# Optimization experiments

Hardware: AMD Instinct MI355X
Metric: run time of the kernel (lower is better)

The kernel has to match this reference:

```python
import jax, jax.numpy as jnp
import numpy as np

N, C, T, V = 32, 64, 512, 21
INTER = 16  # out_channels // coff_embedding(4)
EPS = 1e-5


def _build_A():
    # 21-joint skeleton, spatial strategy: [self(identity), inward, outward], column-normalized
    parents = [-1, 0, 1, 2, 3, 1, 5, 6, 1, 8, 9, 0, 11, 12, 13, 0, 15, 16, 17, 7, 10]
    inw = np.zeros((V, V), np.float32)
    for i, p in enumerate(parents):
        if p >= 0:
            inw[i, p] = 1.0

    def norm(a):
        d = a.sum(0)
        return a * np.where(d > 0, 1.0 / d, 0.0).astype(np.float32)

    I = np.eye(V, dtype=np.float32)
    return np.stack([norm(I), norm(inw), norm(inw.T)]).astype(np.float32)


def setup_inputs():
    key = jax.random.key(0)
    k = jax.random.split(key, 24)
    rn = lambda i, s: jax.random.normal(k[i], s, jnp.float32)
    A = jnp.asarray(_build_A())
    return dict(
        x=rn(0, (N, C, T, V)),
        A=A,
        bn1_gamma=1.0 + 0.1 * rn(1, (C * V,)),
        bn1_beta=0.1 * rn(2, (C * V,)),
        bn1_mean=0.05 * rn(3, (C * V,)),
        bn1_var=jnp.ones((C * V,), jnp.float32),
        PA=A,
        alpha=rn(4, (1,)),
        wa=0.05 * rn(5, (3, INTER, C)), ba=0.05 * rn(6, (3, INTER)),
        wb=0.05 * rn(7, (3, INTER, C)), bb=0.05 * rn(8, (3, INTER)),
        wd=0.05 * rn(9, (3, C, C)), bd=0.05 * rn(10, (3, C)),
        bn2_gamma=1.0 + 0.1 * rn(11, (C,)),
        bn2_beta=0.1 * rn(12, (C,)),
        bn2_mean=0.05 * rn(13, (C,)),
        bn2_var=jnp.ones((C,), jnp.float32),
        w_sa=0.05 * rn(14, (1, C, V)), b_sa=0.05 * rn(15, (1,)),
        w_ta=0.05 * rn(16, (1, C, 9)), b_ta=0.05 * rn(17, (1,)),
        w_fc1=0.05 * rn(18, (C // 2, C)), b_fc1=0.05 * rn(19, (C // 2,)),
        w_fc2=0.05 * rn(20, (C, C // 2)), b_fc2=0.05 * rn(21, (C,)),
    )


def _conv1d(z, w, b):
    pad = (w.shape[2] - 1) // 2
    y = jax.lax.conv_general_dilated(z, w, (1,), [(pad, pad)],
                                     dimension_numbers=('NCH', 'OIH', 'NCH'))
    return y + b[None, :, None]


def reference(x, A, bn1_gamma, bn1_beta, bn1_mean, bn1_var, PA, alpha,
              wa, ba, wb, bb, wd, bd, bn2_gamma, bn2_beta, bn2_mean, bn2_var,
              w_sa, b_sa, w_ta, b_ta, w_fc1, b_fc1, w_fc2, b_fc2):
    n, c, t, v = x.shape
    # data_bn: (N,C,T,V) -> (N,V,T,C) -> raw reshape (N,V*C,T), BN1d, back to (N,C,T,V)
    xb = x.transpose(0, 3, 2, 1).reshape(n, v * c, t)
    scale1 = (bn1_gamma / jnp.sqrt(bn1_var + EPS))
    xb = (xb - bn1_mean[None, :, None]) * scale1[None, :, None] + bn1_beta[None, :, None]
    xb = xb.reshape(n, v, c, t).transpose(0, 2, 3, 1)  # (N,C,T,V)

    e = wa.shape[1]
    # attention embeddings, vectorized over the 3 subsets (s)
    a1 = (jnp.einsum('nctv,sec->nsvet', xb, wa) + ba[None, :, None, :, None]).reshape(n, 3, v, e * t)
    a2 = (jnp.einsum('nctv,sec->nsetv', xb, wb) + bb[None, :, :, None, None]).reshape(n, 3, e * t, v)
    attn = jnp.tanh(jnp.matmul(a1, a2) / float(e * t))  # (N,3,V,V)
    adj = PA[None] + attn * alpha[0]
    # graph aggregation: (N,1,C*T,V) @ (N,3,V,V)
    xz = jnp.matmul(xb.reshape(n, 1, c * t, v), adj).reshape(n, 3, c, t, v)
    y = jnp.einsum('nsctv,soc->notv', xz, wd) + bd.sum(0)[None, :, None, None]

    scale2 = (bn2_gamma / jnp.sqrt(bn2_var + EPS))
    y = (y - bn2_mean[None, :, None, None]) * scale2[None, :, None, None] + bn2_beta[None, :, None, None]
    y = jax.nn.relu(y + xb)  # residual (in==out -> identity down)

    # spatial attention
    se = y.mean(2)  # (N,C,V)
    y = y * jax.nn.sigmoid(_conv1d(se, w_sa, b_sa))[:, :, None, :] + y
    # temporal attention
    se = y.mean(3)  # (N,C,T)
    y = y * jax.nn.sigmoid(_conv1d(se, w_ta, b_ta))[:, :, :, None] + y
    # channel attention
    se = y.mean((2, 3))  # (N,C)
    se2 = jax.nn.sigmoid(jax.nn.relu(se @ w_fc1.T + b_fc1) @ w_fc2.T + b_fc2)
    y = y * se2[:, :, None, None] + y
    return jax.nn.relu(y)
```

## Files before the change

kernel.cpp:

```cpp
#include <hip/hip_runtime.h>
#include <hip/hip_bf16.h>
#include <math.h>


#define Nn 32
#define Cc 64
#define Tt 512
#define Vv 21
#define VP 24
#define Ss 3
#define EPSf 1e-5f
#define NCHUNK 16
#define SVV (Ss*Vv*Vv)
#define KSTR 136

typedef __attribute__((ext_vector_type(8))) short short8;
typedef __attribute__((ext_vector_type(4))) float f32x4;

__device__ __forceinline__ float sigm(float x){ return 1.f/(1.f+expf(-x)); }
__device__ __forceinline__ float bf2f(unsigned short u){ return __uint_as_float((unsigned)u << 16); }
__device__ __forceinline__ unsigned short f2bf(float f){
    __hip_bfloat16 h = __float2bfloat16(f);
    return *reinterpret_cast<unsigned short*>(&h);
}

__global__ __launch_bounds__(256) void k_xb(
    const float* __restrict__ x,
    const float* __restrict__ g1, const float* __restrict__ b1,
    const float* __restrict__ mu1, const float* __restrict__ var1,
    unsigned short* __restrict__ xbT)
{
    const int c0 = blockIdx.x & 63;
    const int ah = blockIdx.x >> 6;
    const int n  = blockIdx.y;
    const int tid = threadIdx.x;
    __shared__ float brick[256*24];
    __shared__ float2 pps[32*26];

    const float* xs = x + (size_t)(n*64 + c0)*10752 + ah*5376;
    for (int i = tid; i < 1344; i += 256){
        float4 d = *reinterpret_cast<const float4*>(xs + i*4);
        int f = i*4;
        #pragma unroll
        for (int e = 0; e < 4; ++e){
            int fe = f + e;
            int t = fe / 21;
            int v = fe - t*21;
            brick[t*24 + v] = ((const float*)&d)[e];
        }
    }
    for (int i = tid; i < 768; i += 256){
        int al = i / 24, vp = i % 24;
        float2 p = make_float2(0.f, 0.f);
        if (vp < 21){
            int j = vp*64 + ah*32 + al;
            float sc = g1[j]*rsqrtf(var1[j]+EPSf);
            p.x = sc; p.y = b1[j] - mu1[j]*sc;
        }
        pps[al*26 + vp] = p;
    }
    __syncthreads();

    #pragma unroll
    for (int ii = 0; ii < 3; ++ii){
        int i = tid + ii*256;
        int vp  = i % 24;
        int m   = (i / 24) % 8;
        int agl = i / 192;
        unsigned short pk[8];
        #pragma unroll
        for (int da = 0; da < 8; ++da){
            int al = agl*8 + da;
            float val = 0.f;
            if (vp < 21){
                float xv = brick[(al*8 + m)*24 + vp];
                float2 p = pps[al*26 + vp];
                val = xv*p.x + p.y;
            }
            pk[da] = f2bf(val);
        }
        *reinterpret_cast<uint4*>(
            xbT + ((size_t)((n*512 + c0 + 64*m)*24 + vp))*64 + ah*32 + agl*8) =
            *reinterpret_cast<const uint4*>(pk);
    }
}

__global__ __launch_bounds__(256) void k_wdT(
    const float* __restrict__ wd, const float* __restrict__ bd,
    const float* __restrict__ g2, const float* __restrict__ b2,
    const float* __restrict__ mu2, const float* __restrict__ var2,
    unsigned short* __restrict__ wdF, float4* __restrict__ bn2p)
{
    int i = blockIdx.x*256 + threadIdx.x;
    if (i < 1536){
        int s  = i / 512;
        int w  = (i >> 7) & 3;
        int ks = (i >> 6) & 1;
        int l  = i & 63;
        int o  = 16*w + (l & 15);
        #pragma unroll
        for (int j = 0; j < 8; ++j){
            int c = 32*ks + 8*(l >> 4) + j;
            wdF[(size_t)i*8 + j] = f2bf(wd[(s*64 + o)*64 + c]);
        }
    }
    if (i < 64){
        float bsum = bd[i] + bd[64+i] + bd[128+i];
        float sc = g2[i]*rsqrtf(var2[i]+EPSf);
        bn2p[i] = make_float4(bsum, sc, mu2[i], b2[i]);
    }
}

__global__ __launch_bounds__(256) void k_wab(
    const float* __restrict__ wa, const float* __restrict__ wb,
    unsigned short* __restrict__ wawbF)
{
    int i = blockIdx.x*256 + threadIdx.x;
    if (i >= 768) return;
    int mt = i / 128;
    int ks = (i / 64) & 1;
    int l  = i & 63;
    int e  = l & 15;
    int g  = l >> 4;
    const float* src = (mt < 3) ? wa : wb;
    int s = (mt < 3) ? mt : mt - 3;
    #pragma unroll
    for (int j = 0; j < 8; ++j){
        int c = ks*32 + 8*g + j;
        wawbF[(size_t)i*8 + j] = f2bf(src[(s*16 + e)*64 + c]);
    }
}

__global__ __launch_bounds__(256) void k_attn(
    const unsigned short* __restrict__ xbT,
    const unsigned short* __restrict__ wawbF,
    const float* __restrict__ ba, const float* __restrict__ bb,
    float* __restrict__ part)
{
    const int chunk = blockIdx.x;
    const int n = blockIdx.y;
    const int tid = threadIdx.x;
    const int w  = tid >> 6;
    const int l  = tid & 63;
    const int g  = l >> 4;
    const int ln = l & 15;

    __shared__ unsigned short m1buf[3*32*KSTR];
    __shared__ unsigned short m2buf[3*32*KSTR];

    for (int i = tid; i < 3*8*KSTR; i += 256){
        int s = i / (8*KSTR), r = i % (8*KSTR);
        int off = (s*32 + 24)*KSTR + r;
        m1buf[off] = 0; m2buf[off] = 0;
    }

    short8 aF[6][2];
    float4 bias4[6];
    #pragma unroll
    for (int mt = 0; mt < 6; ++mt){
        #pragma unroll
        for (int ks = 0; ks < 2; ++ks)
            aF[mt][ks] = *reinterpret_cast<const short8*>(wawbF + (size_t)((mt*2+ks)*64 + l)*8);
        const float* bsrc = (mt < 3) ? (ba + mt*16) : (bb + (mt-3)*16);
        bias4[mt] = *reinterpret_cast<const float4*>(bsrc + 4*g);
    }

    f32x4 accB[3];
    #pragma unroll
    for (int q = 0; q < 3; ++q) accB[q] = (f32x4){0.f,0.f,0.f,0.f};

    int colv[3], colt[3];
    #pragma unroll
    for (int q = 0; q < 3; ++q){
        int col = (3*w + q)*16 + ln;
        colt[q] = col / 24;
        colv[q] = col % 24;
    }

    for (int st = 0; st < 4; ++st){
        const int tb = chunk*32 + st*8;
        #pragma unroll
        for (int q = 0; q < 3; ++q){
            const unsigned short* bp = xbT + ((size_t)(n*512 + tb + colt[q])*24 + colv[q])*64;
            short8 b0 = *reinterpret_cast<const short8*>(bp + 8*g);
            short8 b1 = *reinterpret_cast<const short8*>(bp + 32 + 8*g);
            #pragma unroll
            for (int mt = 0; mt < 6; ++mt){
                f32x4 c;
                c[0] = bias4[mt].x; c[1] = bias4[mt].y;
                c[2] = bias4[mt].z; c[3] = bias4[mt].w;
                c = __builtin_amdgcn_mfma_f32_16x16x32_bf16(aF[mt][0], b0, c, 0, 0, 0);
                c = __builtin_amdgcn_mfma_f32_16x16x32_bf16(aF[mt][1], b1, c, 0, 0, 0);
                unsigned short* dst = (mt < 3) ? m1buf : m2buf;
                int s = (mt < 3) ? mt : mt - 3;
                unsigned u0 = (unsigned)f2bf(c[0]) | ((unsigned)f2bf(c[1]) << 16);
                unsigned u1 = (unsigned)f2bf(c[2]) | ((unsigned)f2bf(c[3]) << 16);
                int off = (s*32 + colv[q])*KSTR + colt[q]*16 + 4*g;
                *reinterpret_cast<uint2*>(dst + off) = make_uint2(u0, u1);
            }
        }
        __syncthreads();
        #pragma unroll
        for (int q = 0; q < 3; ++q){
            int ct = 3*w + q;
            int s = ct >> 2, mtile = (ct >> 1) & 1, ntile = ct & 1;
            #pragma unroll
            for (int kk = 0; kk < 4; ++kk){
                short8 a = *reinterpret_cast<const short8*>(&m1buf[(s*32 + mtile*16 + ln)*KSTR + kk*32 + 8*g]);
                short8 b = *reinterpret_cast<const short8*>(&m2buf[(s*32 + ntile*16 + ln)*KSTR + kk*32 + 8*g]);
                accB[q] = __builtin_amdgcn_mfma_f32_16x16x32_bf16(a, b, accB[q], 0, 0, 0);
            }
        }
        __syncthreads();
    }

    float* pout = part + (size_t)(n*NCHUNK + chunk)*SVV;
    #pragma unroll
    for (int q = 0; q < 3; ++q){
        int ct = 3*w + q;
        int s = ct >> 2, mtile = (ct >> 1) & 1, ntile = ct & 1;
        int v = ntile*16 + ln;
        #pragma unroll
        for (int r = 0; r < 4; ++r){
            int u = mtile*16 + 4*g + r;
            if (u < 21 && v < 21)
                pout[s*441 + u*21 + v] = accB[q][r];
        }
    }
}

__global__ void k_adj(const float* __restrict__ part, const float* __restrict__ PA,
                      const float* __restrict__ alpha, float* __restrict__ adj)
{
    int i = blockIdx.x*256 + threadIdx.x;
    if (i >= Nn*SVV) return;
    int n = i / SVV;
    int idx = i % SVV;
    float pre = 0.f;
    for (int ch = 0; ch < NCHUNK; ++ch)
        pre += part[(size_t)(n*NCHUNK+ch)*SVV + idx];
    adj[i] = PA[idx] + tanhf(pre * (1.f/8192.f)) * alpha[0];
}

__global__ __launch_bounds__(256) void k_adjF(const float* __restrict__ adj,
                                              unsigned short* __restrict__ adjF)
{
    int i = blockIdx.x*256 + threadIdx.x;
    if (i >= Nn*Ss*2*64) return;
    int n = i / 384;
    int r = i % 384;
    int s = r / 128;
    int r2 = r % 128;
    int h = r2 >> 6;
    int l = r2 & 63;
    int v = 16*h + (l & 15);
    #pragma unroll
    for (int j = 0; j < 8; ++j){
        int u = 8*(l >> 4) + j;
        float val = (u < 21 && v < 21) ? adj[(size_t)n*SVV + s*441 + u*21 + v] : 0.f;
        adjF[(size_t)i*8 + j] = f2bf(val);
    }
}

__global__ __launch_bounds__(256) void k_y0(
    const unsigned short* __restrict__ xbT,
    const unsigned short* __restrict__ adjF,
    const unsigned short* __restrict__ wdF,
    const float4* __restrict__ bn2p,
    float* __restrict__ y0)
{
    const int n  = blockIdx.y;
    const int t0 = blockIdx.x * 4;
    const int tid = threadIdx.x;
    const int w  = tid >> 6;
    const int l  = tid & 63;
    const int g  = l >> 4;
    const int ln = l & 15;

    __shared__ unsigned short xbuf[64*136];
    __shared__ unsigned short zbuf[128*72];

    {
        int c = tid >> 2, t = tid & 3;
        *reinterpret_cast<uint4*>(&xbuf[c*136 + t*32 + 24]) = make_uint4(0u,0u,0u,0u);
    }
    for (int k = 0; k < 3; ++k){
        int i = tid + k*256;
        int u = i % 24, t = (i/24) & 3, cg = i / 96;
        uint4 d = *reinterpret_cast<const uint4*>(
            xbT + ((size_t)(n*512 + t0 + t)*24 + u)*64 + cg*8);
        const unsigned short* p = reinterpret_cast<const unsigned short*>(&d);
        #pragma unroll
        for (int dc = 0; dc < 8; ++dc)
            xbuf[(cg*8 + dc)*136 + t*32 + u] = p[dc];
    }
    __syncthreads();

    short8 ax[4];
    #pragma unroll
    for (int t = 0; t < 4; ++t)
        ax[t] = *reinterpret_cast<const short8*>(&xbuf[(16*w + ln)*136 + t*32 + 8*g]);

    short8 badj[3][2];
    {
        const unsigned short* ap = adjF + (size_t)n*Ss*2*64*8;
        #pragma unroll
        for (int s = 0; s < 3; ++s)
            #pragma unroll
            for (int h = 0; h < 2; ++h)
                badj[s][h] = *reinterpret_cast<const short8*>(ap + ((s*2 + h)*64 + l)*8);
    }

    f32x4 acc[8];
    #pragma unroll
    for (int ct = 0; ct < 8; ++ct) acc[ct] = (f32x4){0.f,0.f,0.f,0.f};

    for (int s = 0; s < 3; ++s){
        if (s) __syncthreads();
        f32x4 dz[8];
        #pragma unroll
        for (int ct = 0; ct < 8; ++ct)
            dz[ct] = __builtin_amdgcn_mfma_f32_16x16x32_bf16(
                         ax[ct>>1], badj[s][ct&1], (f32x4){0.f,0.f,0.f,0.f}, 0, 0, 0);
        #pragma unroll
        for (int ct = 0; ct < 8; ++ct){
            unsigned u0 = (unsigned)f2bf(dz[ct][0]) | ((unsigned)f2bf(dz[ct][1]) << 16);
            unsigned u1 = (unsigned)f2bf(dz[ct][2]) | ((unsigned)f2bf(dz[ct][3]) << 16);
            int col = (ct >> 1)*32 + (ct & 1)*16 + ln;
            *reinterpret_cast<uint2*>(&zbuf[col*72 + 16*w + 4*g]) = make_uint2(u0, u1);
        }
        __syncthreads();
        short8 aw0 = *reinterpret_cast<const short8*>(wdF + (size_t)(((s*4 + w)*2 + 0)*64 + l)*8);
        short8 aw1 = *reinterpret_cast<const short8*>(wdF + (size_t)(((s*4 + w)*2 + 1)*64 + l)*8);
        #pragma unroll
        for (int ct = 0; ct < 8; ++ct){
            int col = (ct >> 1)*32 + (ct & 1)*16 + ln;
            short8 b0 = *reinterpret_cast<const short8*>(&zbuf[col*72 + 0  + 8*g]);
            short8 b1 = *reinterpret_cast<const short8*>(&zbuf[col*72 + 32 + 8*g]);
            acc[ct] = __builtin_amdgcn_mfma_f32_16x16x32_bf16(aw0, b0, acc[ct], 0, 0, 0);
            acc[ct] = __builtin_amdgcn_mfma_f32_16x16x32_bf16(aw1, b1, acc[ct], 0, 0, 0);
        }
    }

    float4 bp[4];
    #pragma unroll
    for (int r = 0; r < 4; ++r) bp[r] = bn2p[16*w + 4*g + r];
    #pragma unroll
    for (int ct = 0; ct < 8; ++ct){
        const int t  = ct >> 1;
        const int vp = (ct & 1)*16 + ln;
        if (vp < 21){
            #pragma unroll
            for (int r = 0; r < 4; ++r){
                const int o = 16*w + 4*g + r;
                float val = acc[ct][r] + bp[r].x;
                val = (val - bp[r].z)*bp[r].y + bp[r].w;
                val += bf2f(xbuf[o*136 + t*32 + vp]);
                y0[((size_t)(n*64 + o)*512 + t0 + t)*21 + vp] = fmaxf(val, 0.f);
            }
        }
    }
}

__global__ __launch_bounds__(256) void k_M1(const float* __restrict__ y0, float* __restrict__ M1)
{
    const int c = blockIdx.x, n = blockIdx.y, tid = threadIdx.x;
    float a[21];
    #pragma unroll
    for (int v = 0; v < 21; ++v) a[v] = 0.f;
    for (int t = tid; t < Tt; t += 256){
        const float* p = &y0[ ((size_t)(n*Cc+c)*Tt + t)*Vv ];
        #pragma unroll
        for (int v = 0; v < 21; ++v) a[v] += p[v];
    }
    __shared__ float red[256][21];
    #pragma unroll
    for (int v = 0; v < 21; ++v) red[tid][v] = a[v];
    __syncthreads();
    for (int off = 128; off > 0; off >>= 1){
        if (tid < off){
            #pragma unroll
            for (int v = 0; v < 21; ++v) red[tid][v] += red[tid+off][v];
        }
        __syncthreads();
    }
    if (tid < 21) M1[(size_t)(n*Cc+c)*Vv + tid] = red[0][tid];
}

__global__ __launch_bounds__(256) void k_s1(const float* __restrict__ M1, const float* __restrict__ w_sa,
                     const float* __restrict__ b_sa, float* __restrict__ s1)
{
    const int n = blockIdx.x, tid = threadIdx.x;
    __shared__ float m1s[64][22];
    __shared__ float ws[64][22];
    __shared__ float red[12][21];
    for (int i = tid; i < 1344; i += 256){
        int c = i / 21, v = i % 21;
        m1s[c][v] = M1[(size_t)(n*64+c)*21 + v];
        ws[c][v]  = w_sa[i];
    }
    __syncthreads();
    const int v = tid % 21;
    const int cg = tid / 21;
    float sum = 0.f;
    if (tid < 252){
        for (int c = cg; c < 64; c += 12){
            #pragma unroll
            for (int k = 0; k < 21; ++k){
                int src = v + k - 10;
                if (src >= 0 && src < 21)
                    sum += m1s[c][src] * ws[c][k];
            }
        }
        red[cg][v] = sum;
    }
    __syncthreads();
    if (tid < 21){
        float tot = b_sa[0];
        #pragma unroll
        for (int g = 0; g < 12; ++g) tot += red[g][tid] * (1.f/512.f);
        s1[n*Vv + tid] = 1.f + sigm(tot);
    }
}

__global__ __launch_bounds__(256) void k_M2(const float* __restrict__ y0, const float* __restrict__ s1,
                      float* __restrict__ M2)
{
    int t = blockIdx.x*256 + threadIdx.x;
    int nc = blockIdx.y;
    int n = nc >> 6;
    __shared__ float s1s[21];
    if (threadIdx.x < 21) s1s[threadIdx.x] = s1[n*Vv + threadIdx.x];
    __syncthreads();
    const float* p = &y0[ ((size_t)nc*Tt + t)*Vv ];
    float sum = 0.f;
    #pragma unroll
    for (int v = 0; v < 21; ++v) sum += p[v]*s1s[v];
    M2[(size_t)nc*Tt + t] = sum;
}

__global__ __launch_bounds__(256) void k_s2(const float* __restrict__ M2, const float* __restrict__ w_ta,
                      const float* __restrict__ b_ta, float* __restrict__ s2)
{
    const int n = blockIdx.y;
    const int t0 = blockIdx.x * 64;
    const int tid = threadIdx.x;
    __shared__ float m2s[64][72];
    __shared__ float wts[576];
    __shared__ float red[4][64];
    for (int i = tid; i < 64*72; i += 256){
        int c = i / 72, tt = i % 72;
        int src = t0 + tt - 4;
        m2s[c][tt] = (src >= 0 && src < 512) ? M2[(size_t)(n*64+c)*512 + src] : 0.f;
    }
    for (int i = tid; i < 576; i += 256) wts[i] = w_ta[i];
    __syncthreads();
    const int tl = tid & 63;
    const int cg = tid >> 6;
    float sum = 0.f;
    for (int c = cg*16; c < cg*16+16; ++c){
        #pragma unroll
        for (int k = 0; k < 9; ++k)
            sum += m2s[c][tl + k] * wts[c*9 + k];
    }
    red[cg][tl] = sum;
    __syncthreads();
    if (cg == 0){
        float tot = b_ta[0] + (red[0][tl]+red[1][tl]+red[2][tl]+red[3][tl]) * (1.f/21.f);
        s2[n*512 + t0 + tl] = 1.f + sigm(tot);
    }
}

__global__ __launch_bounds__(256) void k_sec(const float* __restrict__ M2, const float* __restrict__ s2,
                      float* __restrict__ sec)
{
    const int c = blockIdx.x, n = blockIdx.y, tid = threadIdx.x;
    const float* row = &M2[(size_t)(n*Cc+c)*Tt];
    const float* s2r = &s2[n*Tt];
    float acc = row[tid]*s2r[tid] + row[tid+256]*s2r[tid+256];
    #pragma unroll
    for (int off = 32; off > 0; off >>= 1)
        acc += __shfl_down(acc, off, 64);
    __shared__ float red[4];
    if ((tid & 63) == 0) red[tid >> 6] = acc;
    __syncthreads();
    if (tid == 0)
        sec[n*Cc + c] = (red[0]+red[1]+red[2]+red[3]) * (1.f/(512.f*21.f));
}

__global__ __launch_bounds__(64) void k_s3fc(const float* __restrict__ sec,
                     const float* __restrict__ w1, const float* __restrict__ bf1,
                     const float* __restrict__ w2, const float* __restrict__ bf2,
                     float* __restrict__ s3)
{
    int n = blockIdx.x, c = threadIdx.x;
    __shared__ float secs[64];
    __shared__ float hh[32];
    secs[c] = sec[n*Cc + c];
    __syncthreads();
    if (c < 32){
        float h = bf1[c];
        #pragma unroll 8
        for (int k = 0; k < 64; ++k) h += w1[c*64+k]*secs[k];
        hh[c] = fmaxf(h, 0.f);
    }
    __syncthreads();
    float o = bf2[c];
    #pragma unroll 8
    for (int k = 0; k < 32; ++k) o += w2[c*32+k]*hh[k];
    s3[n*Cc + c] = 1.f + sigm(o);
}

__global__ __launch_bounds__(256) void k_final(float* __restrict__ y,
    const float* __restrict__ s1, const float* __restrict__ s2, const float* __restrict__ s3)
{
    const int c = blockIdx.x, n = blockIdx.y, tid = threadIdx.x;
    __shared__ float s1s[21];
    __shared__ float s2s[512];
    if (tid < 21) s1s[tid] = s1[n*Vv + tid];
    for (int i = tid; i < 512; i += 256) s2s[i] = s2[n*512 + i];
    __syncthreads();
    const float sc3 = s3[n*Cc + c];
    float* base = y + (size_t)(n*Cc + c)*10752;
    for (int i = tid; i < 2688; i += 256){
        float4 d = *reinterpret_cast<const float4*>(base + i*4);
        float r[4];
        #pragma unroll
        for (int e = 0; e < 4; ++e){
            int f = i*4 + e;
            int t = f / 21;
            int v = f - t*21;
            r[e] = fmaxf(((const float*)&d)[e] * s1s[v] * s2s[t] * sc3, 0.f);
        }
        *reinterpret_cast<float4*>(base + i*4) = make_float4(r[0], r[1], r[2], r[3]);
    }
}

extern "C" void kernel_launch(void* const* d_in, const int* in_sizes, int n_in,
                              void* d_out, int out_size, void* d_ws, size_t ws_size,
                              hipStream_t stream)
{
    const float* x    = (const float*)d_in[0];
    const float* g1   = (const float*)d_in[2];
    const float* b1   = (const float*)d_in[3];
    const float* mu1  = (const float*)d_in[4];
    const float* var1 = (const float*)d_in[5];
    const float* PA   = (const float*)d_in[6];
    const float* alpha= (const float*)d_in[7];
    const float* wa   = (const float*)d_in[8];
    const float* ba   = (const float*)d_in[9];
    const float* wb   = (const float*)d_in[10];
    const float* bb   = (const float*)d_in[11];
    const float* wd   = (const float*)d_in[12];
    const float* bd   = (const float*)d_in[13];
    const float* g2   = (const float*)d_in[14];
    const float* b2   = (const float*)d_in[15];
    const float* mu2  = (const float*)d_in[16];
    const float* var2 = (const float*)d_in[17];
    const float* w_sa = (const float*)d_in[18];
    const float* b_sa = (const float*)d_in[19];
    const float* w_ta = (const float*)d_in[20];
    const float* b_ta = (const float*)d_in[21];
    const float* w_fc1= (const float*)d_in[22];
    const float* b_fc1= (const float*)d_in[23];
    const float* w_fc2= (const float*)d_in[24];
    const float* b_fc2= (const float*)d_in[25];

    unsigned short* xbT = (unsigned short*)d_ws;
    float* fws  = (float*)d_ws + 12582912;
    float* part = fws;
    float* adjw = part + 677376;
    float* M1   = adjw + 42336;
    float* s1   = M1   + 43008;
    float* M2   = s1   + 672;
    float* s2   = M2   + 1048576;
    float* s3   = s2   + 16384;
    float4* bn2p = (float4*)(s3 + 2048);
    unsigned short* wdF   = (unsigned short*)((float*)bn2p + 256);
    unsigned short* adjF  = wdF + 12288;
    unsigned short* wawbF = adjF + 98304;
    float* sec  = (float*)(wawbF + 6144);
    float* y0   = (float*)d_out;

    k_xb  <<<dim3(128, Nn), 256, 0, stream>>>(x, g1,b1,mu1,var1, xbT);
    k_wdT <<<6, 256, 0, stream>>>(wd, bd, g2, b2, mu2, var2, wdF, bn2p);
    k_wab <<<3, 256, 0, stream>>>(wa, wb, wawbF);
    k_attn<<<dim3(NCHUNK, Nn), 256, 0, stream>>>(xbT, wawbF, ba, bb, part);
    k_adj <<<(Nn*SVV + 255)/256, 256, 0, stream>>>(part, PA, alpha, adjw);
    k_adjF<<<48, 256, 0, stream>>>(adjw, adjF);
    k_y0  <<<dim3(Tt/4, Nn), 256, 0, stream>>>(xbT, adjF, wdF, bn2p, y0);
    k_M1  <<<dim3(Cc, Nn), 256, 0, stream>>>(y0, M1);
    k_s1  <<<Nn, 256, 0, stream>>>(M1, w_sa, b_sa, s1);
    k_M2  <<<dim3(Tt/256, Nn*Cc), 256, 0, stream>>>(y0, s1, M2);
    k_s2  <<<dim3(8, Nn), 256, 0, stream>>>(M2, w_ta, b_ta, s2);
    k_sec <<<dim3(Cc, Nn), 256, 0, stream>>>(M2, s2, sec);
    k_s3fc<<<Nn, 64, 0, stream>>>(sec, w_fc1, b_fc1, w_fc2, b_fc2, s3);
    k_final<<<dim3(Cc, Nn), 256, 0, stream>>>(y0, s1, s2, s3);
}
```

Before: 199.2 us.

## Restage k_xb with full-row bf16 LDS brick and 64-channel vectorized stores

The xb normalization/transpose kernel now has each block load a full 10752-float slab (both halves) and store it in shared memory as bf16 in a 32-wide swizzled layout. The BN scale and offset are precomputed for all 64 columns, and 192 threads each write eight 16-byte packed outputs. The goal is to halve the block count, cut shared memory footprint, avoid bank conflicts and make global stores contiguous across a 64-wide row. In exchange, 64 of the 256 threads sit idle in the output phase, and the input is rounded to bf16 before the BN affine is applied, which adds a small precision change.

```diff
diff --git a/kernel.cpp b/kernel.cpp
--- a/kernel.cpp
+++ b/kernel.cpp
@@ -30,58 +30,55 @@
     const float* __restrict__ mu1, const float* __restrict__ var1,
     unsigned short* __restrict__ xbT)
 {
-    const int c0 = blockIdx.x & 63;
-    const int ah = blockIdx.x >> 6;
+    const int c0 = blockIdx.x;
     const int n  = blockIdx.y;
     const int tid = threadIdx.x;
-    __shared__ float brick[256*24];
-    __shared__ float2 pps[32*26];
-
-    const float* xs = x + (size_t)(n*64 + c0)*10752 + ah*5376;
-    for (int i = tid; i < 1344; i += 256){
+    __shared__ unsigned short brick16[512*32];
+    __shared__ float scs[21*65], ofs[21*65];
+
+    for (int j = tid; j < 1344; j += 256){
+        int vp = j >> 6, a = j & 63;
+        float sc = g1[j]*rsqrtf(var1[j]+EPSf);
+        scs[vp*65 + a] = sc;
+        ofs[vp*65 + a] = b1[j] - mu1[j]*sc;
+    }
+    const float* xs = x + (size_t)(n*64 + c0)*10752;
+    for (int i = tid; i < 2688; i += 256){
         float4 d = *reinterpret_cast<const float4*>(xs + i*4);
-        int f = i*4;
         #pragma unroll
         for (int e = 0; e < 4; ++e){
-            int fe = f + e;
-            int t = fe / 21;
-            int v = fe - t*21;
-            brick[t*24 + v] = ((const float*)&d)[e];
-        }
-    }
-    for (int i = tid; i < 768; i += 256){
-        int al = i / 24, vp = i % 24;
-        float2 p = make_float2(0.f, 0.f);
-        if (vp < 21){
-            int j = vp*64 + ah*32 + al;
-            float sc = g1[j]*rsqrtf(var1[j]+EPSf);
-            p.x = sc; p.y = b1[j] - mu1[j]*sc;
-        }
-        pps[al*26 + vp] = p;
-    }
-    __syncthreads();
-
-    #pragma unroll
-    for (int ii = 0; ii < 3; ++ii){
-        int i = tid + ii*256;
-        int vp  = i % 24;
-        int m   = (i / 24) % 8;
-        int agl = i / 192;
-        unsigned short pk[8];
+            int f = i*4 + e;
+            int t = f / 21;
+            int v = f - t*21;
+            brick16[t*32 + ((v + 8*(t>>6)) & 31)] = f2bf(((const float*)&d)[e]);
+        }
+    }
+    __syncthreads();
+
+    if (tid < 192){
+        const int agl = tid & 7;
+        const int vp  = tid >> 3;
+        const bool valid = (vp < 21);
+        float scr[8], ofr[8];
         #pragma unroll
         for (int da = 0; da < 8; ++da){
-            int al = agl*8 + da;
-            float val = 0.f;
-            if (vp < 21){
-                float xv = brick[(al*8 + m)*24 + vp];
-                float2 p = pps[al*26 + vp];
-                val = xv*p.x + p.y;
+            scr[da] = valid ? scs[vp*65 + agl*8 + da] : 0.f;
+            ofr[da] = valid ? ofs[vp*65 + agl*8 + da] : 0.f;
+        }
+        unsigned short* ob = xbT + ((size_t)(n*512 + c0)*24 + vp)*64 + agl*8;
+        #pragma unroll
+        for (int m = 0; m < 8; ++m){
+            unsigned short pk[8];
+            #pragma unroll
+            for (int da = 0; da < 8; ++da){
+                int row = agl*64 + da*8 + m;
+                float xv = bf2f(brick16[row*32 + ((vp + 8*agl) & 31)]);
+                float r = xv*scr[da] + ofr[da];
+                pk[da] = valid ? f2bf(r) : (unsigned short)0;
             }
-            pk[da] = f2bf(val);
-        }
-        *reinterpret_cast<uint4*>(
-            xbT + ((size_t)((n*512 + c0 + 64*m)*24 + vp))*64 + ah*32 + agl*8) =
-            *reinterpret_cast<const uint4*>(pk);
+            *reinterpret_cast<uint4*>(ob + (size_t)m*64*24*64) =
+                *reinterpret_cast<const uint4*>(pk);
+        }
     }
 }
 
@@ -582,7 +579,7 @@
     float* sec  = (float*)(wawbF + 6144);
     float* y0   = (float*)d_out;
 
-    k_xb  <<<dim3(128, Nn), 256, 0, stream>>>(x, g1,b1,mu1,var1, xbT);
+    k_xb  <<<dim3(64, Nn), 256, 0, stream>>>(x, g1,b1,mu1,var1, xbT);
     k_wdT <<<6, 256, 0, stream>>>(wd, bd, g2, b2, mu2, var2, wdF, bn2p);
     k_wab <<<3, 256, 0, stream>>>(wa, wb, wawbF);
     k_attn<<<dim3(NCHUNK, Nn), 256, 0, stream>>>(xbT, wawbF, ba, bb, part);
```

Result: faster. 179.5 us (-9.9%).
